# Kernel optimization log

Measured on AMD Instinct MI355X. Metric: run time of the kernel, lower is better.

The kernel has to match this reference:

```python
import jax, jax.numpy as jnp
import numpy as np

ADMP = 16  # admp_channel


def _backbone(x, Wc, bc):
    # Conv2d(3->256, k=3, stride=2, pad=1) + ReLU stands in for feature_backbone
    y = jax.lax.conv_general_dilated(x, Wc, window_strides=(2, 2),
                                     padding=((1, 1), (1, 1)),
                                     dimension_numbers=('NCHW', 'OIHW', 'NCHW'))
    return jax.nn.relu(y + bc[None, :, None, None])


def _feature_select(feat, k):
    # AdaptiveMaxPool2d(k, return_indices=True) on feat.sum(1); H,W divisible by k
    B, C, H, W = feat.shape
    bh, bw = H // k, W // k
    resp = feat.sum(1)  # [B,H,W]
    r = resp.reshape(B, k, bh, k, bw).transpose(0, 1, 3, 2, 4).reshape(B, k, k, bh * bw)
    loc = jnp.argmax(r, axis=-1)            # local flat index in each bh*bw block
    lr, lc = loc // bw, loc % bw
    rows = jnp.arange(k)[None, :, None] * bh + lr   # [B,k,k]
    cols = jnp.arange(k)[None, None, :] * bw + lc
    return (rows * W + cols).reshape(B, k * k)      # flat indices into H*W


def _mlp(x, W1, b1, W2, b2):
    # Linear -> ReLU -> (Dropout eval = identity) -> Linear
    return jax.nn.relu(x @ W1 + b1) @ W2 + b2


def reference(xA, xB, Wconv, bconv, W1r, b1r, W2r, b2r, W1c, b1c, W2c, b2c):
    fA = _backbone(xA, Wconv, bconv)  # [B,C,H,W]
    fB = _backbone(xB, Wconv, bconv)
    B, C, H, W = fA.shape
    N = H * W
    idxA = _feature_select(fA, ADMP)                       # [B,K]
    fA_flat = fA.reshape(B, C, N)
    fB_flat = fB.reshape(B, C, N)
    desc = jnp.take_along_axis(fA_flat, idxA[:, None, :], axis=2)  # [B,C,K]
    # ||a-b||^2 = ||a||^2 - 2 a.b + ||b||^2 ; fused batched kNN
    dist = ((desc ** 2).sum(1)[:, :, None]
            - 2.0 * jnp.einsum('bck,bcn->bkn', desc, fB_flat)
            + (fB_flat ** 2).sum(1)[:, None, :])           # [B,K,N]
    minidx = jnp.argmin(dist, axis=-1)                     # [B,K]
    # original uses high (==width here since H==W) for both div and mod
    row_A, col_A = idxA // H, idxA % H
    row_B, col_B = minidx // H, minidx % H
    drow = (row_B - row_A).astype(jnp.float32)             # [B,K]
    dcol = (col_A - col_B).astype(jnp.float32)
    out_drow = _mlp(drow, W1r, b1r, W2r, b2r)              # [B,1]
    out_dcol = _mlp(dcol, W1c, b1c, W2c, b2c)
    return jnp.concatenate([out_drow, out_dcol], axis=1)   # [B,2]


def setup_inputs() -> dict:
    key = jax.random.key(0)
    ks = jax.random.split(key, 8)
    K2 = ADMP * ADMP
    return {
        'xA': jax.random.normal(ks[0], (4, 3, 256, 256), jnp.float32),
        'xB': jax.random.normal(ks[1], (4, 3, 256, 256), jnp.float32),
        'Wconv': jax.random.normal(ks[2], (256, 3, 3, 3), jnp.float32) * 0.1,
        'bconv': jnp.zeros((256,), jnp.float32),
        'W1r': jax.random.normal(ks[3], (K2, K2 // 2), jnp.float32) * 0.05,
        'b1r': jnp.zeros((K2 // 2,), jnp.float32),
        'W2r': jax.random.normal(ks[4], (K2 // 2, 1), jnp.float32) * 0.05,
        'b2r': jnp.zeros((1,), jnp.float32),
        'W1c': jax.random.normal(ks[5], (K2, K2 // 2), jnp.float32) * 0.05,
        'b1c': jnp.zeros((K2 // 2,), jnp.float32),
        'W2c': jax.random.normal(ks[6], (K2 // 2, 1), jnp.float32) * 0.05,
        'b2c': jnp.zeros((1,), jnp.float32),
    }
```

## Files before the change

kernel.cpp:

```cpp
#include <hip/hip_runtime.h>
#include <stdint.h>

constexpr int NB   = 4;
constexpr int CIN  = 3;
constexpr int HIN  = 256;
constexpr int COUT = 256;
constexpr int HF   = 128;
constexpr int NF   = HF * HF;
constexpr int KADM = 16;
constexpr int KK   = KADM * KADM;
constexpr int HID  = 128;
constexpr int DFB  = 65536;

typedef unsigned short ushort_t;
typedef __attribute__((ext_vector_type(8))) _Float16 f16x8;
typedef __attribute__((ext_vector_type(4))) float    f32x4;

__device__ inline unsigned long long shfl_xor_u64(unsigned long long v, int m) {
    unsigned lo = __shfl_xor((unsigned)v, m, 64);
    unsigned hi = __shfl_xor((unsigned)(v >> 32), m, 64);
    return ((unsigned long long)hi << 32) | lo;
}
__device__ inline unsigned long long shfl_down_u64(unsigned long long v, int off) {
    unsigned lo = __shfl_down((unsigned)v, off, 64);
    unsigned hi = __shfl_down((unsigned)(v >> 32), off, 64);
    return ((unsigned long long)hi << 32) | lo;
}
__device__ inline unsigned long long u64min(unsigned long long a, unsigned long long b) {
    return a < b ? a : b;
}
__device__ inline ushort_t f16bits(_Float16 h) { return __builtin_bit_cast(ushort_t, h); }

__device__ inline int swz(int pix, int c) {
    return pix * 256 + ((((c >> 3) ^ (pix & 7)) << 3) | (c & 7));
}

__device__ inline int dfoff(int w, int chunk, int j, int lane) {
    return (((w * 8 + chunk) * 4 + j) * 64 + lane) * 8;
}

__global__ __launch_bounds__(256) void prep_kernel(
        const float* __restrict__ W, ushort_t* __restrict__ WFh, ushort_t* __restrict__ WFl)
{
    int co = threadIdx.x;
    int w = co >> 6, j = (co >> 4) & 3, la = co & 15;
    #pragma unroll
    for (int q = 0; q < 32; ++q) {
        float v = (q < 27) ? W[co * 27 + q] : 0.f;
        _Float16 h = (_Float16)v;
        _Float16 l = (_Float16)(v - (float)h);
        int lg = q >> 3, e = q & 7;
        int off = ((w * 4 + j) * 64 + lg * 16 + la) * 8 + e;
        WFh[off] = f16bits(h);
        WFl[off] = f16bits(l);
    }
}

__global__ __launch_bounds__(256) void convA_kernel(
        const float* __restrict__ xA,
        const ushort_t* __restrict__ WFh, const ushort_t* __restrict__ WFl,
        const float* __restrict__ bias, float* __restrict__ resp)
{
    __shared__ float    pS[CIN][3][132];
    __shared__ ushort_t Ah[64][40];
    __shared__ ushort_t Al[64][40];
    __shared__ float    redS[4][64];

    int tile = blockIdx.x;
    int b    = blockIdx.y;
    int oh   = tile >> 1;
    int ow0  = (tile & 1) << 6;
    const float* x = xA + (size_t)b * CIN * HIN * HIN;
    int tid = threadIdx.x;

    for (int i = tid; i < CIN * 3 * 129; i += 256) {
        int ci = i / (3 * 129);
        int r2 = i % (3 * 129);
        int kh = r2 / 129, c = r2 % 129;
        int gr = 2 * oh - 1 + kh, gc = 2 * ow0 - 1 + c;
        float v = 0.f;
        if (gr >= 0 && gr < HIN && gc >= 0 && gc < HIN)
            v = x[(size_t)ci * HIN * HIN + (size_t)gr * HIN + gc];
        pS[ci][kh][c] = v;
    }
    __syncthreads();

    {
        int n = tid >> 2, qg = tid & 3;
        unsigned uh[4], ul[4];
        #pragma unroll
        for (int e2 = 0; e2 < 4; ++e2) {
            ushort_t hh[2], ll[2];
            #pragma unroll
            for (int s = 0; s < 2; ++s) {
                int q = qg * 8 + e2 * 2 + s;
                float v = 0.f;
                if (q < 27) {
                    int ci = q / 9, r = (q % 9) / 3, kw = q % 3;
                    v = pS[ci][r][2 * n + kw];
                }
                _Float16 h = (_Float16)v;
                _Float16 l = (_Float16)(v - (float)h);
                hh[s] = f16bits(h); ll[s] = f16bits(l);
            }
            uh[e2] = (unsigned)hh[0] | ((unsigned)hh[1] << 16);
            ul[e2] = (unsigned)ll[0] | ((unsigned)ll[1] << 16);
        }
        *(uint4*)&Ah[n][qg * 8] = *(uint4*)uh;
        *(uint4*)&Al[n][qg * 8] = *(uint4*)ul;
    }
    __syncthreads();

    int lane = tid & 63, w = tid >> 6;
    int la = lane & 15, lg = lane >> 4;
    int wbase = w * 64;

    float bj[4];
    #pragma unroll
    for (int j = 0; j < 4; ++j) bj[j] = bias[wbase + j * 16 + la];

    f16x8 ah[4], al[4], bh[4], bl[4];
    #pragma unroll
    for (int i = 0; i < 4; ++i) {
        ah[i] = *(const f16x8*)&Ah[i * 16 + la][lg * 8];
        al[i] = *(const f16x8*)&Al[i * 16 + la][lg * 8];
    }
    #pragma unroll
    for (int j = 0; j < 4; ++j) {
        int off = ((w * 4 + j) * 64 + lane) * 8;
        bh[j] = *(const f16x8*)&WFh[off];
        bl[j] = *(const f16x8*)&WFl[off];
    }

    f32x4 acc[4][4];
    #pragma unroll
    for (int i = 0; i < 4; ++i)
        #pragma unroll
        for (int j = 0; j < 4; ++j) acc[i][j] = (f32x4)0.f;

    #pragma unroll
    for (int i = 0; i < 4; ++i)
        #pragma unroll
        for (int j = 0; j < 4; ++j) {
            acc[i][j] = __builtin_amdgcn_mfma_f32_16x16x32_f16(ah[i], bh[j], acc[i][j], 0, 0, 0);
            acc[i][j] = __builtin_amdgcn_mfma_f32_16x16x32_f16(al[i], bh[j], acc[i][j], 0, 0, 0);
            acc[i][j] = __builtin_amdgcn_mfma_f32_16x16x32_f16(ah[i], bl[j], acc[i][j], 0, 0, 0);
        }

    float s[4][4];
    #pragma unroll
    for (int i = 0; i < 4; ++i)
        #pragma unroll
        for (int r = 0; r < 4; ++r) s[i][r] = 0.f;

    #pragma unroll
    for (int i = 0; i < 4; ++i)
        #pragma unroll
        for (int j = 0; j < 4; ++j)
            #pragma unroll
            for (int r = 0; r < 4; ++r)
                s[i][r] += fmaxf(acc[i][j][r] + bj[j], 0.f);

    #pragma unroll
    for (int i = 0; i < 4; ++i)
        #pragma unroll
        for (int r = 0; r < 4; ++r) {
            float v = s[i][r];
            v += __shfl_xor(v, 1, 64);
            v += __shfl_xor(v, 2, 64);
            v += __shfl_xor(v, 4, 64);
            v += __shfl_xor(v, 8, 64);
            s[i][r] = v;
        }
    if (la == 0) {
        #pragma unroll
        for (int i = 0; i < 4; ++i)
            #pragma unroll
            for (int r = 0; r < 4; ++r)
                redS[w][i * 16 + lg * 4 + r] = s[i][r];
    }
    __syncthreads();
    if (tid < 64) {
        float tot = redS[0][tid] + redS[1][tid] + redS[2][tid] + redS[3][tid];
        resp[(size_t)b * NF + oh * HF + ow0 + tid] = tot;
    }
}

__global__ __launch_bounds__(256) void select_kernel(
        const float* __restrict__ resp,
        const float* __restrict__ xA, const float* __restrict__ W,
        const float* __restrict__ bias,
        int* __restrict__ idxA,
        ushort_t* __restrict__ dFh, ushort_t* __restrict__ dFl,
        float* __restrict__ normA)
{
    __shared__ float patch[27];
    __shared__ float red[4];
    __shared__ int   sidx;

    int bk = blockIdx.x;
    int b = bk >> 8, k = bk & 255;
    int t = threadIdx.x;

    if (t < 64) {
        int kr = k >> 4, kc = k & 15;
        int lr = t >> 3, lc = t & 7;
        int row = kr * 8 + lr, col = kc * 8 + lc;
        float bv = resp[(size_t)b * NF + (size_t)row * HF + col];
        int best = t;
        for (int off = 32; off > 0; off >>= 1) {
            float ov = __shfl_down(bv, off, 64);
            int   oi = __shfl_down(best, off, 64);
            if (ov > bv || (ov == bv && oi < best)) { bv = ov; best = oi; }
        }
        if (t == 0) {
            int r = kr * 8 + (best >> 3), c = kc * 8 + (best & 7);
            int idx = r * HF + c;
            idxA[bk] = idx;
            sidx = idx;
        }
    }
    __syncthreads();
    int idx = sidx;
    int oh = idx >> 7, ow = idx & 127;

    if (t < 27) {
        int ci = t / 9, kh = (t % 9) / 3, kw = t % 3;
        int ir = oh * 2 - 1 + kh, ic = ow * 2 - 1 + kw;
        float v = 0.f;
        if (ir >= 0 && ir < HIN && ic >= 0 && ic < HIN)
            v = xA[((size_t)b * CIN + ci) * HIN * HIN + (size_t)ir * HIN + ic];
        patch[t] = v;
    }
    __syncthreads();

    float v = bias[t];
    const float* w = &W[t * 27];
    #pragma unroll
    for (int q = 0; q < 27; ++q) v = fmaf(patch[q], w[q], v);
    v = fmaxf(v, 0.f);

    _Float16 h = (_Float16)v;
    _Float16 l = (_Float16)(v - (float)h);
    {
        int wq = k >> 6, j = (k >> 4) & 3, la = k & 15;
        int chunk = t >> 5, lg = (t >> 3) & 3, e = t & 7;
        int off = b * DFB + dfoff(wq, chunk, j, lg * 16 + la) + e;
        dFh[off] = f16bits(h);
        dFl[off] = f16bits(l);
    }

    float s = v * v;
    for (int off = 32; off > 0; off >>= 1) s += __shfl_down(s, off, 64);
    if ((t & 63) == 0) red[t >> 6] = s;
    __syncthreads();
    if (t == 0) normA[bk] = red[0] + red[1] + red[2] + red[3];
}

__device__ inline void load_desc(const ushort_t* __restrict__ dFh,
                                 const ushort_t* __restrict__ dFl,
                                 int w, int chunk, int lane,
                                 f16x8* bh, f16x8* bl)
{
    #pragma unroll
    for (int j = 0; j < 4; ++j) {
        int off = dfoff(w, chunk, j, lane);
        bh[j] = *(const f16x8*)&dFh[off];
        bl[j] = *(const f16x8*)&dFl[off];
    }
}

__device__ inline void knn_chunk(const ushort_t* __restrict__ fH,
                                 const ushort_t* __restrict__ fL,
                                 int la, int lg, int cc,
                                 const f16x8* bh, const f16x8* bl,
                                 f32x4 (&acc)[4][4])
{
    #pragma unroll
    for (int i = 0; i < 4; ++i) {
        f16x8 ah = *(const f16x8*)&fH[swz(i * 16 + la, cc + lg * 8)];
        f16x8 al = *(const f16x8*)&fL[swz(i * 16 + la, cc + lg * 8)];
        __builtin_amdgcn_s_setprio(1);
        #pragma unroll
        for (int j = 0; j < 4; ++j) {
            acc[i][j] = __builtin_amdgcn_mfma_f32_16x16x32_f16(ah, bh[j], acc[i][j], 0, 0, 0);
            acc[i][j] = __builtin_amdgcn_mfma_f32_16x16x32_f16(al, bh[j], acc[i][j], 0, 0, 0);
            acc[i][j] = __builtin_amdgcn_mfma_f32_16x16x32_f16(ah, bl[j], acc[i][j], 0, 0, 0);
        }
        __builtin_amdgcn_s_setprio(0);
    }
}

__global__ __launch_bounds__(256) void fused_kernel(
        const float* __restrict__ xB,
        const ushort_t* __restrict__ WFh, const ushort_t* __restrict__ WFl,
        const float* __restrict__ bias,
        const ushort_t* __restrict__ dFhg, const ushort_t* __restrict__ dFlg,
        const float* __restrict__ normA,
        unsigned long long* __restrict__ scratch)
{
    __shared__ __align__(16) char smem[2 * 64 * 256 * 2];
    __shared__ float redS[4][64];
    __shared__ float nAS[KK];
    __shared__ float nBS[64];

    float*    pSp = (float*)smem;
    ushort_t* AhP = (ushort_t*)(smem + 4752);
    ushort_t* AlP = (ushort_t*)(smem + 4752 + 5120);
    ushort_t* fH  = (ushort_t*)smem;
    ushort_t* fL  = (ushort_t*)(smem + 64 * 256 * 2);

    int tile = blockIdx.x;
    int b    = blockIdx.y;
    int oh   = tile >> 1;
    int ow0  = (tile & 1) << 6;
    const float* x = xB + (size_t)b * CIN * HIN * HIN;
    int tid = threadIdx.x;

    nAS[tid] = normA[b * KK + tid];

    for (int i = tid; i < CIN * 3 * 129; i += 256) {
        int ci = i / (3 * 129);
        int r2 = i % (3 * 129);
        int kh = r2 / 129, c = r2 % 129;
        int gr = 2 * oh - 1 + kh, gc = 2 * ow0 - 1 + c;
        float v = 0.f;
        if (gr >= 0 && gr < HIN && gc >= 0 && gc < HIN)
            v = x[(size_t)ci * HIN * HIN + (size_t)gr * HIN + gc];
        pSp[ci * 3 * 132 + kh * 132 + c] = v;
    }
    __syncthreads();

    {
        int n = tid >> 2, qg = tid & 3;
        unsigned uh[4], ul[4];
        #pragma unroll
        for (int e2 = 0; e2 < 4; ++e2) {
            ushort_t hh[2], ll[2];
            #pragma unroll
            for (int s = 0; s < 2; ++s) {
                int q = qg * 8 + e2 * 2 + s;
                float v = 0.f;
                if (q < 27) {
                    int ci = q / 9, r = (q % 9) / 3, kw = q % 3;
                    v = pSp[ci * 3 * 132 + r * 132 + 2 * n + kw];
                }
                _Float16 h = (_Float16)v;
                _Float16 l = (_Float16)(v - (float)h);
                hh[s] = f16bits(h); ll[s] = f16bits(l);
            }
            uh[e2] = (unsigned)hh[0] | ((unsigned)hh[1] << 16);
            ul[e2] = (unsigned)ll[0] | ((unsigned)ll[1] << 16);
        }
        *(uint4*)&AhP[n * 40 + qg * 8] = *(uint4*)uh;
        *(uint4*)&AlP[n * 40 + qg * 8] = *(uint4*)ul;
    }
    __syncthreads();

    int lane = tid & 63, w = tid >> 6;
    int la = lane & 15, lg = lane >> 4;
    int wbase = w * 64;

    float bj[4];
    #pragma unroll
    for (int j = 0; j < 4; ++j) bj[j] = bias[wbase + j * 16 + la];

    f16x8 cah[4], cal[4], cbh[4], cbl[4];
    #pragma unroll
    for (int i = 0; i < 4; ++i) {
        cah[i] = *(const f16x8*)&AhP[(i * 16 + la) * 40 + lg * 8];
        cal[i] = *(const f16x8*)&AlP[(i * 16 + la) * 40 + lg * 8];
    }
    #pragma unroll
    for (int j = 0; j < 4; ++j) {
        int off = ((w * 4 + j) * 64 + lane) * 8;
        cbh[j] = *(const f16x8*)&WFh[off];
        cbl[j] = *(const f16x8*)&WFl[off];
    }

    f32x4 cacc[4][4];
    #pragma unroll
    for (int i = 0; i < 4; ++i)
        #pragma unroll
        for (int j = 0; j < 4; ++j) cacc[i][j] = (f32x4)0.f;

    #pragma unroll
    for (int i = 0; i < 4; ++i)
        #pragma unroll
        for (int j = 0; j < 4; ++j) {
            cacc[i][j] = __builtin_amdgcn_mfma_f32_16x16x32_f16(cah[i], cbh[j], cacc[i][j], 0, 0, 0);
            cacc[i][j] = __builtin_amdgcn_mfma_f32_16x16x32_f16(cal[i], cbh[j], cacc[i][j], 0, 0, 0);
            cacc[i][j] = __builtin_amdgcn_mfma_f32_16x16x32_f16(cah[i], cbl[j], cacc[i][j], 0, 0, 0);
        }

    __syncthreads();

    float s[4][4];
    #pragma unroll
    for (int i = 0; i < 4; ++i)
        #pragma unroll
        for (int r = 0; r < 4; ++r) s[i][r] = 0.f;

    #pragma unroll
    for (int i = 0; i < 4; ++i) {
        #pragma unroll
        for (int j = 0; j < 4; ++j) {
            int co = wbase + j * 16 + la;
            #pragma unroll
            for (int r = 0; r < 4; ++r) {
                float v = fmaxf(cacc[i][j][r] + bj[j], 0.f);
                _Float16 h = (_Float16)v;
                _Float16 l = (_Float16)(v - (float)h);
                int pix = i * 16 + lg * 4 + r;
                fH[swz(pix, co)] = f16bits(h);
                fL[swz(pix, co)] = f16bits(l);
                s[i][r] = fmaf(v, v, s[i][r]);
            }
        }
    }
    #pragma unroll
    for (int i = 0; i < 4; ++i)
        #pragma unroll
        for (int r = 0; r < 4; ++r) {
            float v = s[i][r];
            v += __shfl_xor(v, 1, 64);
            v += __shfl_xor(v, 2, 64);
            v += __shfl_xor(v, 4, 64);
            v += __shfl_xor(v, 8, 64);
            s[i][r] = v;
        }
    if (la == 0) {
        #pragma unroll
        for (int i = 0; i < 4; ++i)
            #pragma unroll
            for (int r = 0; r < 4; ++r)
                redS[w][i * 16 + lg * 4 + r] = s[i][r];
    }
    __syncthreads();
    if (tid < 64) nBS[tid] = redS[0][tid] + redS[1][tid] + redS[2][tid] + redS[3][tid];
    __syncthreads();

    const ushort_t* dFh = dFhg + (size_t)b * DFB;
    const ushort_t* dFl = dFlg + (size_t)b * DFB;

    f32x4 acc[4][4];
    #pragma unroll
    for (int i = 0; i < 4; ++i)
        #pragma unroll
        for (int j = 0; j < 4; ++j) acc[i][j] = (f32x4)0.f;

    f16x8 bhA[4], blA[4], bhB[4], blB[4];
    load_desc(dFh, dFl, w, 0, lane, bhA, blA);
    load_desc(dFh, dFl, w, 1, lane, bhB, blB);
    knn_chunk(fH, fL, la, lg, 0, bhA, blA, acc);
    load_desc(dFh, dFl, w, 2, lane, bhA, blA);
    knn_chunk(fH, fL, la, lg, 32, bhB, blB, acc);
    load_desc(dFh, dFl, w, 3, lane, bhB, blB);
    knn_chunk(fH, fL, la, lg, 64, bhA, blA, acc);
    load_desc(dFh, dFl, w, 4, lane, bhA, blA);
    knn_chunk(fH, fL, la, lg, 96, bhB, blB, acc);
    load_desc(dFh, dFl, w, 5, lane, bhB, blB);
    knn_chunk(fH, fL, la, lg, 128, bhA, blA, acc);
    load_desc(dFh, dFl, w, 6, lane, bhA, blA);
    knn_chunk(fH, fL, la, lg, 160, bhB, blB, acc);
    load_desc(dFh, dFl, w, 7, lane, bhB, blB);
    knn_chunk(fH, fL, la, lg, 192, bhA, blA, acc);
    knn_chunk(fH, fL, la, lg, 224, bhB, blB, acc);

    float nBv[4][4];
    #pragma unroll
    for (int i = 0; i < 4; ++i) {
        f32x4 t4 = *(const f32x4*)&nBS[i * 16 + lg * 4];
        nBv[i][0] = t4[0]; nBv[i][1] = t4[1]; nBv[i][2] = t4[2]; nBv[i][3] = t4[3];
    }
    int n0 = tile * 64;
    #pragma unroll
    for (int j = 0; j < 4; ++j) {
        int kl = wbase + j * 16 + la;
        float nAv = nAS[kl];
        unsigned long long best = ~0ull;
        #pragma unroll
        for (int i = 0; i < 4; ++i)
            #pragma unroll
            for (int r = 0; r < 4; ++r) {
                int n = n0 + i * 16 + lg * 4 + r;
                float d = fmaf(-2.f, acc[i][j][r], nAv) + nBv[i][r];
                unsigned u = __float_as_uint(d);
                u = (u & 0x80000000u) ? ~u : (u | 0x80000000u);
                unsigned long long key = ((unsigned long long)u << 32) | (unsigned)n;
                best = u64min(best, key);
            }
        best = u64min(best, shfl_xor_u64(best, 16));
        best = u64min(best, shfl_xor_u64(best, 32));
        if (lg == 0)
            scratch[(size_t)(b * KK + kl) * 256 + tile] = best;
    }
}

__global__ __launch_bounds__(64) void reduce_kernel(
        const unsigned long long* __restrict__ scratch, int* __restrict__ minN)
{
    int bk = blockIdx.x;
    int t = threadIdx.x;
    const unsigned long long* s = scratch + (size_t)bk * 256;
    unsigned long long best = s[t];
    best = u64min(best, s[t + 64]);
    best = u64min(best, s[t + 128]);
    best = u64min(best, s[t + 192]);
    for (int off = 32; off > 0; off >>= 1)
        best = u64min(best, shfl_down_u64(best, off));
    if (t == 0) minN[bk] = (int)(best & 0xffffffffULL);
}

__global__ __launch_bounds__(128) void mlp_kernel(
        const int* __restrict__ idxA, const int* __restrict__ minN,
        const float* __restrict__ W1r, const float* __restrict__ b1r,
        const float* __restrict__ W2r, const float* __restrict__ b2r,
        const float* __restrict__ W1c, const float* __restrict__ b1c,
        const float* __restrict__ W2c, const float* __restrict__ b2c,
        float* __restrict__ out)
{
    __shared__ float xS[KK];
    __shared__ float red[2];
    int blk = blockIdx.x;
    int b = blk >> 1, which = blk & 1;
    int t = threadIdx.x;

    for (int k = t; k < KK; k += 128) {
        int ia = idxA[b * KK + k];
        int nn = minN[b * KK + k];
        int rowA = ia >> 7, colA = ia & 127;
        int rowB = nn >> 7, colB = nn & 127;
        xS[k] = (which == 0) ? (float)(rowB - rowA) : (float)(colA - colB);
    }
    __syncthreads();

    const float* W1 = which ? W1c : W1r;
    const float* b1 = which ? b1c : b1r;
    const float* W2 = which ? W2c : W2r;
    const float* b2 = which ? b2c : b2r;

    float h = b1[t];
    for (int k = 0; k < KK; ++k) h = fmaf(xS[k], W1[k * HID + t], h);
    h = fmaxf(h, 0.f);
    float pv = h * W2[t];
    for (int off = 32; off > 0; off >>= 1) pv += __shfl_down(pv, off, 64);
    if ((t & 63) == 0) red[t >> 6] = pv;
    __syncthreads();
    if (t == 0) out[b * 2 + which] = red[0] + red[1] + b2[0];
}

extern "C" void kernel_launch(void* const* d_in, const int* in_sizes, int n_in,
                              void* d_out, int out_size, void* d_ws, size_t ws_size,
                              hipStream_t stream)
{
    const float* xA  = (const float*)d_in[0];
    const float* xB  = (const float*)d_in[1];
    const float* Wc  = (const float*)d_in[2];
    const float* bc  = (const float*)d_in[3];
    const float* W1r = (const float*)d_in[4];
    const float* b1r = (const float*)d_in[5];
    const float* W2r = (const float*)d_in[6];
    const float* b2r = (const float*)d_in[7];
    const float* W1c = (const float*)d_in[8];
    const float* b1c = (const float*)d_in[9];
    const float* W2c = (const float*)d_in[10];
    const float* b2c = (const float*)d_in[11];
    float* out = (float*)d_out;

    char* ws = (char*)d_ws;
    unsigned long long* scratch = (unsigned long long*)ws; ws += (size_t)NB * KK * 256 * 8;
    int*   idxA   = (int*)ws;      ws += (size_t)NB * KK * 4;
    int*   minN   = (int*)ws;      ws += (size_t)NB * KK * 4;
    float* normA  = (float*)ws;    ws += (size_t)NB * KK * 4;
    float* resp   = (float*)ws;    ws += (size_t)NB * NF * 4;
    ushort_t* dFh = (ushort_t*)ws; ws += (size_t)NB * DFB * 2;
    ushort_t* dFl = (ushort_t*)ws; ws += (size_t)NB * DFB * 2;
    ushort_t* WFh = (ushort_t*)ws; ws += (size_t)COUT * 32 * 2;
    ushort_t* WFl = (ushort_t*)ws; ws += (size_t)COUT * 32 * 2;

    prep_kernel  <<<1, 256, 0, stream>>>(Wc, WFh, WFl);
    convA_kernel <<<dim3(256, NB), 256, 0, stream>>>(xA, WFh, WFl, bc, resp);
    select_kernel<<<NB * KK, 256, 0, stream>>>(resp, xA, Wc, bc, idxA, dFh, dFl, normA);
    fused_kernel <<<dim3(256, NB), 256, 0, stream>>>(xB, WFh, WFl, bc, dFh, dFl,
                                                     normA, scratch);
    reduce_kernel<<<NB * KK, 64, 0, stream>>>(scratch, minN);
    mlp_kernel   <<<8, 128, 0, stream>>>(idxA, minN,
                                         W1r, b1r, W2r, b2r,
                                         W1c, b1c, W2c, b2c, out);
}
```

Before: 69.06 us.

## Halve fused kernel pixel tile to 32 and double grid blocks

Shrinks the per-block pixel tile in the fused conv+kNN kernel from 64 to 32 pixels, which doubles the grid to 512 blocks per batch and halves shared memory and accumulator registers per block. It also adds a launch-bounds occupancy hint and issues the first descriptor loads before the norm reduction so they overlap it. The aim is more resident blocks per CU to hide latency. The cost is that descriptor loads from global memory are amortised over fewer pixels, and the reduce kernel now has twice as many partial minima to combine.

```diff
diff --git a/kernel.cpp b/kernel.cpp
--- a/kernel.cpp
+++ b/kernel.cpp
@@ -11,6 +11,8 @@
 constexpr int KK   = KADM * KADM;
 constexpr int HID  = 128;
 constexpr int DFB  = 65536;
+constexpr int PX   = 32;
+constexpr int NT   = NF / PX;
 
 typedef unsigned short ushort_t;
 typedef __attribute__((ext_vector_type(8))) _Float16 f16x8;
@@ -274,10 +276,10 @@
                                  const ushort_t* __restrict__ fL,
                                  int la, int lg, int cc,
                                  const f16x8* bh, const f16x8* bl,
-                                 f32x4 (&acc)[4][4])
-{
-    #pragma unroll
-    for (int i = 0; i < 4; ++i) {
+                                 f32x4 (&acc)[2][4])
+{
+    #pragma unroll
+    for (int i = 0; i < 2; ++i) {
         f16x8 ah = *(const f16x8*)&fH[swz(i * 16 + la, cc + lg * 8)];
         f16x8 al = *(const f16x8*)&fL[swz(i * 16 + la, cc + lg * 8)];
         __builtin_amdgcn_s_setprio(1);
@@ -291,7 +293,7 @@
     }
 }
 
-__global__ __launch_bounds__(256) void fused_kernel(
+__global__ __launch_bounds__(256, 4) void fused_kernel(
         const float* __restrict__ xB,
         const ushort_t* __restrict__ WFh, const ushort_t* __restrict__ WFl,
         const float* __restrict__ bias,
@@ -299,61 +301,60 @@
         const float* __restrict__ normA,
         unsigned long long* __restrict__ scratch)
 {
-    __shared__ __align__(16) char smem[2 * 64 * 256 * 2];
-    __shared__ float redS[4][64];
+    __shared__ __align__(16) char smem[2 * PX * 256 * 2];
+    __shared__ float redS[4][PX];
     __shared__ float nAS[KK];
-    __shared__ float nBS[64];
+    __shared__ float nBS[PX];
 
     float*    pSp = (float*)smem;
-    ushort_t* AhP = (ushort_t*)(smem + 4752);
-    ushort_t* AlP = (ushort_t*)(smem + 4752 + 5120);
+    ushort_t* AhP = (ushort_t*)(smem + 2448);
+    ushort_t* AlP = (ushort_t*)(smem + 2448 + 2560);
     ushort_t* fH  = (ushort_t*)smem;
-    ushort_t* fL  = (ushort_t*)(smem + 64 * 256 * 2);
+    ushort_t* fL  = (ushort_t*)(smem + PX * 256 * 2);
 
     int tile = blockIdx.x;
     int b    = blockIdx.y;
-    int oh   = tile >> 1;
-    int ow0  = (tile & 1) << 6;
+    int oh   = tile >> 2;
+    int ow0  = (tile & 3) << 5;
     const float* x = xB + (size_t)b * CIN * HIN * HIN;
     int tid = threadIdx.x;
 
     nAS[tid] = normA[b * KK + tid];
 
-    for (int i = tid; i < CIN * 3 * 129; i += 256) {
-        int ci = i / (3 * 129);
-        int r2 = i % (3 * 129);
-        int kh = r2 / 129, c = r2 % 129;
+    for (int i = tid; i < CIN * 3 * 65; i += 256) {
+        int ci = i / (3 * 65);
+        int r2 = i % (3 * 65);
+        int kh = r2 / 65, c = r2 % 65;
         int gr = 2 * oh - 1 + kh, gc = 2 * ow0 - 1 + c;
         float v = 0.f;
         if (gr >= 0 && gr < HIN && gc >= 0 && gc < HIN)
             v = x[(size_t)ci * HIN * HIN + (size_t)gr * HIN + gc];
-        pSp[ci * 3 * 132 + kh * 132 + c] = v;
+        pSp[ci * 204 + kh * 68 + c] = v;
     }
     __syncthreads();
 
     {
-        int n = tid >> 2, qg = tid & 3;
-        unsigned uh[4], ul[4];
-        #pragma unroll
-        for (int e2 = 0; e2 < 4; ++e2) {
-            ushort_t hh[2], ll[2];
-            #pragma unroll
-            for (int s = 0; s < 2; ++s) {
-                int q = qg * 8 + e2 * 2 + s;
-                float v = 0.f;
-                if (q < 27) {
-                    int ci = q / 9, r = (q % 9) / 3, kw = q % 3;
-                    v = pSp[ci * 3 * 132 + r * 132 + 2 * n + kw];
-                }
-                _Float16 h = (_Float16)v;
-                _Float16 l = (_Float16)(v - (float)h);
-                hh[s] = f16bits(h); ll[s] = f16bits(l);
+        int n = tid >> 3, qg = tid & 7;
+        ushort_t hh[4], ll[4];
+        #pragma unroll
+        for (int s = 0; s < 4; ++s) {
+            int q = qg * 4 + s;
+            float v = 0.f;
+            if (q < 27) {
+                int ci = q / 9, r = (q % 9) / 3, kw = q % 3;
+                v = pSp[ci * 204 + r * 68 + 2 * n + kw];
             }
-            uh[e2] = (unsigned)hh[0] | ((unsigned)hh[1] << 16);
-            ul[e2] = (unsigned)ll[0] | ((unsigned)ll[1] << 16);
-        }
-        *(uint4*)&AhP[n * 40 + qg * 8] = *(uint4*)uh;
-        *(uint4*)&AlP[n * 40 + qg * 8] = *(uint4*)ul;
+            _Float16 h = (_Float16)v;
+            _Float16 l = (_Float16)(v - (float)h);
+            hh[s] = f16bits(h); ll[s] = f16bits(l);
+        }
+        unsigned lo, hi;
+        lo = (unsigned)hh[0] | ((unsigned)hh[1] << 16);
+        hi = (unsigned)hh[2] | ((unsigned)hh[3] << 16);
+        *(uint2*)&AhP[n * 40 + qg * 4] = make_uint2(lo, hi);
+        lo = (unsigned)ll[0] | ((unsigned)ll[1] << 16);
+        hi = (unsigned)ll[2] | ((unsigned)ll[3] << 16);
+        *(uint2*)&AlP[n * 40 + qg * 4] = make_uint2(lo, hi);
     }
     __syncthreads();
 
@@ -365,9 +366,9 @@
     #pragma unroll
     for (int j = 0; j < 4; ++j) bj[j] = bias[wbase + j * 16 + la];
 
-    f16x8 cah[4], cal[4], cbh[4], cbl[4];
-    #pragma unroll
-    for (int i = 0; i < 4; ++i) {
+    f16x8 cah[2], cal[2], cbh[4], cbl[4];
+    #pragma unroll
+    for (int i = 0; i < 2; ++i) {
         cah[i] = *(const f16x8*)&AhP[(i * 16 + la) * 40 + lg * 8];
         cal[i] = *(const f16x8*)&AlP[(i * 16 + la) * 40 + lg * 8];
     }
@@ -378,14 +379,14 @@
         cbl[j] = *(const f16x8*)&WFl[off];
     }
 
-    f32x4 cacc[4][4];
-    #pragma unroll
-    for (int i = 0; i < 4; ++i)
+    f32x4 cacc[2][4];
+    #pragma unroll
+    for (int i = 0; i < 2; ++i)
         #pragma unroll
         for (int j = 0; j < 4; ++j) cacc[i][j] = (f32x4)0.f;
 
     #pragma unroll
-    for (int i = 0; i < 4; ++i)
+    for (int i = 0; i < 2; ++i)
         #pragma unroll
         for (int j = 0; j < 4; ++j) {
             cacc[i][j] = __builtin_amdgcn_mfma_f32_16x16x32_f16(cah[i], cbh[j], cacc[i][j], 0, 0, 0);
@@ -395,14 +396,14 @@
 
     __syncthreads();
 
-    float s[4][4];
-    #pragma unroll
-    for (int i = 0; i < 4; ++i)
+    float s[2][4];
+    #pragma unroll
+    for (int i = 0; i < 2; ++i)
         #pragma unroll
         for (int r = 0; r < 4; ++r) s[i][r] = 0.f;
 
     #pragma unroll
-    for (int i = 0; i < 4; ++i) {
+    for (int i = 0; i < 2; ++i) {
         #pragma unroll
         for (int j = 0; j < 4; ++j) {
             int co = wbase + j * 16 + la;
@@ -418,8 +419,15 @@
             }
         }
     }
-    #pragma unroll
-    for (int i = 0; i < 4; ++i)
+
+    const ushort_t* dFh = dFhg + (size_t)b * DFB;
+    const ushort_t* dFl = dFlg + (size_t)b * DFB;
+    f16x8 bhA[4], blA[4], bhB[4], blB[4];
+    load_desc(dFh, dFl, w, 0, lane, bhA, blA);
+    load_desc(dFh, dFl, w, 1, lane, bhB, blB);
+
+    #pragma unroll
+    for (int i = 0; i < 2; ++i)
         #pragma unroll
         for (int r = 0; r < 4; ++r) {
             float v = s[i][r];
@@ -431,27 +439,21 @@
         }
     if (la == 0) {
         #pragma unroll
-        for (int i = 0; i < 4; ++i)
+        for (int i = 0; i < 2; ++i)
             #pragma unroll
             for (int r = 0; r < 4; ++r)
                 redS[w][i * 16 + lg * 4 + r] = s[i][r];
     }
     __syncthreads();
-    if (tid < 64) nBS[tid] = redS[0][tid] + redS[1][tid] + redS[2][tid] + redS[3][tid];
-    __syncthreads();
-
-    const ushort_t* dFh = dFhg + (size_t)b * DFB;
-    const ushort_t* dFl = dFlg + (size_t)b * DFB;
-
-    f32x4 acc[4][4];
-    #pragma unroll
-    for (int i = 0; i < 4; ++i)
+    if (tid < PX) nBS[tid] = redS[0][tid] + redS[1][tid] + redS[2][tid] + redS[3][tid];
+    __syncthreads();
+
+    f32x4 acc[2][4];
+    #pragma unroll
+    for (int i = 0; i < 2; ++i)
         #pragma unroll
         for (int j = 0; j < 4; ++j) acc[i][j] = (f32x4)0.f;
 
-    f16x8 bhA[4], blA[4], bhB[4], blB[4];
-    load_desc(dFh, dFl, w, 0, lane, bhA, blA);
-    load_desc(dFh, dFl, w, 1, lane, bhB, blB);
     knn_chunk(fH, fL, la, lg, 0, bhA, blA, acc);
     load_desc(dFh, dFl, w, 2, lane, bhA, blA);
     knn_chunk(fH, fL, la, lg, 32, bhB, blB, acc);
@@ -467,20 +469,20 @@
     knn_chunk(fH, fL, la, lg, 192, bhA, blA, acc);
     knn_chunk(fH, fL, la, lg, 224, bhB, blB, acc);
 
-    float nBv[4][4];
-    #pragma unroll
-    for (int i = 0; i < 4; ++i) {
+    float nBv[2][4];
+    #pragma unroll
+    for (int i = 0; i < 2; ++i) {
         f32x4 t4 = *(const f32x4*)&nBS[i * 16 + lg * 4];
         nBv[i][0] = t4[0]; nBv[i][1] = t4[1]; nBv[i][2] = t4[2]; nBv[i][3] = t4[3];
     }
-    int n0 = tile * 64;
+    int n0 = tile * PX;
     #pragma unroll
     for (int j = 0; j < 4; ++j) {
         int kl = wbase + j * 16 + la;
         float nAv = nAS[kl];
         unsigned long long best = ~0ull;
         #pragma unroll
-        for (int i = 0; i < 4; ++i)
+        for (int i = 0; i < 2; ++i)
             #pragma unroll
             for (int r = 0; r < 4; ++r) {
                 int n = n0 + i * 16 + lg * 4 + r;
@@ -493,7 +495,7 @@
         best = u64min(best, shfl_xor_u64(best, 16));
         best = u64min(best, shfl_xor_u64(best, 32));
         if (lg == 0)
-            scratch[(size_t)(b * KK + kl) * 256 + tile] = best;
+            scratch[(size_t)(b * KK + kl) * NT + tile] = best;
     }
 }
 
@@ -502,11 +504,11 @@
 {
     int bk = blockIdx.x;
     int t = threadIdx.x;
-    const unsigned long long* s = scratch + (size_t)bk * 256;
-    unsigned long long best = s[t];
-    best = u64min(best, s[t + 64]);
-    best = u64min(best, s[t + 128]);
-    best = u64min(best, s[t + 192]);
+    const unsigned long long* s = scratch + (size_t)bk * NT;
+    unsigned long long best = ~0ull;
+    #pragma unroll
+    for (int m = 0; m < NT / 64; ++m)
+        best = u64min(best, s[t + m * 64]);
     for (int off = 32; off > 0; off >>= 1)
         best = u64min(best, shfl_down_u64(best, off));
     if (t == 0) minN[bk] = (int)(best & 0xffffffffULL);
@@ -569,7 +571,7 @@
     float* out = (float*)d_out;
 
     char* ws = (char*)d_ws;
-    unsigned long long* scratch = (unsigned long long*)ws; ws += (size_t)NB * KK * 256 * 8;
+    unsigned long long* scratch = (unsigned long long*)ws; ws += (size_t)NB * KK * NT * 8;
     int*   idxA   = (int*)ws;      ws += (size_t)NB * KK * 4;
     int*   minN   = (int*)ws;      ws += (size_t)NB * KK * 4;
     float* normA  = (float*)ws;    ws += (size_t)NB * KK * 4;
@@ -582,8 +584,8 @@
     prep_kernel  <<<1, 256, 0, stream>>>(Wc, WFh, WFl);
     convA_kernel <<<dim3(256, NB), 256, 0, stream>>>(xA, WFh, WFl, bc, resp);
     select_kernel<<<NB * KK, 256, 0, stream>>>(resp, xA, Wc, bc, idxA, dFh, dFl, normA);
-    fused_kernel <<<dim3(256, NB), 256, 0, stream>>>(xB, WFh, WFl, bc, dFh, dFl,
-                                                     normA, scratch);
+    fused_kernel <<<dim3(NT, NB), 256, 0, stream>>>(xB, WFh, WFl, bc, dFh, dFl,
+                                                    normA, scratch);
     reduce_kernel<<<NB * KK, 64, 0, stream>>>(scratch, minN);
     mlp_kernel   <<<8, 128, 0, stream>>>(idxA, minN,
                                          W1r, b1r, W2r, b2r,
```

Result: slower. 70.79 us (+2.5%).
